# Performance work log

Hardware: AMD Instinct MI355X
Metric: run time of the kernel (lower is better)

The kernel has to match this reference:

```python
import jax, jax.numpy as jnp
import numpy as np

D_MODEL = 1024
NUM_HEADS = 16
D_K = D_MODEL // NUM_HEADS
THETA = 10000.0
BATCH = 4
SEQ = 2048


def _apply_rope(t, positions, theta):
    # t: (B, H, S, d_k); positions: (S,) int
    d_k = t.shape[-1]
    inv_freq = theta ** (-jnp.arange(0, d_k, 2, dtype=jnp.float32) / d_k)  # (d_k/2,)
    angles = positions.astype(jnp.float32)[:, None] * inv_freq[None, :]    # (S, d_k/2)
    cos = jnp.cos(angles)
    sin = jnp.sin(angles)
    x1 = t[..., 0::2]
    x2 = t[..., 1::2]
    r1 = x1 * cos - x2 * sin
    r2 = x1 * sin + x2 * cos
    # interleave back to (..., d_k)
    return jnp.stack([r1, r2], axis=-1).reshape(t.shape)


def setup_inputs() -> dict:
    key = jax.random.key(0)
    k0, k1, k2, k3, k4 = jax.random.split(key, 5)
    scale = 1.0 / np.sqrt(D_MODEL)
    return {
        "x": jax.random.normal(k0, (BATCH, SEQ, D_MODEL), dtype=jnp.float32),
        "wq": jax.random.normal(k1, (D_MODEL, D_MODEL), dtype=jnp.float32) * scale,
        "wk": jax.random.normal(k2, (D_MODEL, D_MODEL), dtype=jnp.float32) * scale,
        "wv": jax.random.normal(k3, (D_MODEL, D_MODEL), dtype=jnp.float32) * scale,
        "wo": jax.random.normal(k4, (D_MODEL, D_MODEL), dtype=jnp.float32) * scale,
        "token_positions": jnp.arange(SEQ, dtype=jnp.int32),
    }


def reference(x, wq, wk, wv, wo, token_positions):
    B, S, _ = x.shape
    H, dk = NUM_HEADS, D_K

    def proj(w):
        # Linear: y = x @ w.T, then split heads -> (B, H, S, d_k)
        y = jnp.einsum("bsd,ed->bse", x, w)
        return y.reshape(B, S, H, dk).transpose(0, 2, 1, 3)

    q = proj(wq)
    k = proj(wk)
    v = proj(wv)

    q = _apply_rope(q, token_positions, THETA)
    k = _apply_rope(k, token_positions, THETA)

    scores = jnp.einsum("bhqd,bhkd->bhqk", q, k) / jnp.sqrt(jnp.float32(dk))
    causal = jnp.tril(jnp.ones((S, S), dtype=bool))  # (S, S)
    scores = jnp.where(causal[None, None, :, :], scores, -jnp.inf)
    attn = jax.nn.softmax(scores, axis=-1)
    out = jnp.einsum("bhqk,bhkd->bhqd", attn, v)        # (B, H, S, d_k)
    out = out.transpose(0, 2, 1, 3).reshape(B, S, H * dk)
    return jnp.einsum("bse,de->bsd", out, wo)
```

## Files before the change

kernel.cpp:

```cpp
#include <hip/hip_runtime.h>
#include <hip/hip_bf16.h>

#define D_MODEL 1024
#define NHEADS 16
#define DKH 64
#define BATCH 4
#define SEQ 2048
#define BH_ (BATCH*NHEADS)
#define MROWS (BATCH*SEQ)

typedef __attribute__((ext_vector_type(8))) short bf16x8;
typedef __attribute__((ext_vector_type(4))) float f32x4;
typedef __attribute__((ext_vector_type(4))) short short4v;

static __device__ __forceinline__ unsigned short f2b(float f){
  union { float f; unsigned u; } v; v.f = f;
  unsigned u = v.u;
  return (unsigned short)((u + 0x7FFFu + ((u >> 16) & 1u)) >> 16);
}
static __device__ __forceinline__ float b2f(unsigned short h){
  union { unsigned u; float f; } v; v.u = ((unsigned)h) << 16; return v.f;
}

static __device__ __forceinline__ f32x4 mfma16(bf16x8 a, bf16x8 b, f32x4 c){
  return __builtin_amdgcn_mfma_f32_16x16x32_bf16(a, b, c, 0, 0, 0);
}

static __device__ __forceinline__ float fexp2(float x){
#if __has_builtin(__builtin_amdgcn_exp2f)
  return __builtin_amdgcn_exp2f(x);
#else
  float r; asm("v_exp_f32 %0, %1" : "=v"(r) : "v"(x)); return r;
#endif
}

static __device__ __forceinline__ void gload_lds16(const unsigned short* g, void* l){
  __builtin_amdgcn_global_load_lds((const __attribute__((address_space(1))) void*)g,
                                   (__attribute__((address_space(3))) void*)l,
                                   16, 0, 0);
}

__global__ void cvt_bf16_kernel(const float* __restrict__ src,
                                unsigned short* __restrict__ dst, int n4){
  int i = blockIdx.x*blockDim.x + threadIdx.x;
  if (i >= n4) return;
  float4 f = ((const float4*)src)[i];
  short4v o;
  o.x = (short)f2b(f.x); o.y = (short)f2b(f.y);
  o.z = (short)f2b(f.z); o.w = (short)f2b(f.w);
  ((short4v*)dst)[i] = o;
}

__global__ void cvt_w_kernel(const float* __restrict__ wq, const float* __restrict__ wk,
                             const float* __restrict__ wv, const float* __restrict__ wo,
                             unsigned short* __restrict__ wcat, unsigned short* __restrict__ wob){
  int i = blockIdx.x*blockDim.x + threadIdx.x;
  int seg = i >> 18;
  int j = i & 0x3FFFF;
  const float* s = (seg==0) ? wq : (seg==1) ? wk : (seg==2) ? wv : wo;
  unsigned short* d = (seg < 3) ? (wcat + ((size_t)seg << 20)) : wob;
  float4 f = ((const float4*)s)[j];
  short4v o;
  o.x = (short)f2b(f.x); o.y = (short)f2b(f.y);
  o.z = (short)f2b(f.z); o.w = (short)f2b(f.w);
  ((short4v*)d)[j] = o;
}

#define BM 128
#define BN 128
#define BKG 64

template<int MODE>
__global__ __launch_bounds__(256, 3) void gemm_nt(const unsigned short* __restrict__ A,
                                                  const unsigned short* __restrict__ Bw,
                                                  void* __restrict__ C,
                                                  int M, int N, int K)
{
  __shared__ unsigned short As[BM*BKG];
  __shared__ unsigned short Bs[BN*BKG];
  const int t = threadIdx.x;
  const int lane = t & 63;
  const int wv = t >> 6;
  const int wr = wv >> 1, wc = wv & 1;
  const int l15 = lane & 15, l4 = lane >> 4;
  const int m0 = blockIdx.y*BM, n0 = blockIdx.x*BN;

  f32x4 acc[4][4] = {};

  const int srow = lane >> 3;
  const int sce  = (lane & 7) * 8;

  for (int kt = 0; kt < K; kt += BKG){
    __syncthreads();
    #pragma unroll
    for (int jj = 0; jj < 4; ++jj){
      const int i = wv + jj*4;
      const int row = i*8 + srow;
      gload_lds16(A  + (size_t)(m0 + row)*K + kt + sce, (char*)As + i*1024 + lane*16);
      gload_lds16(Bw + (size_t)(n0 + row)*K + kt + sce, (char*)Bs + i*1024 + lane*16);
    }
    __syncthreads();
    #pragma unroll
    for (int kk = 0; kk < 2; ++kk){
      bf16x8 af[4], bfr[4];
      #pragma unroll
      for (int mi = 0; mi < 4; ++mi)
        af[mi] = *(const bf16x8*)((const char*)As + (wr*64 + mi*16 + l15)*128 + kk*64 + l4*16);
      #pragma unroll
      for (int ni = 0; ni < 4; ++ni)
        bfr[ni] = *(const bf16x8*)((const char*)Bs + (wc*64 + ni*16 + l15)*128 + kk*64 + l4*16);
      #pragma unroll
      for (int mi = 0; mi < 4; ++mi)
        #pragma unroll
        for (int ni = 0; ni < 4; ++ni)
          acc[mi][ni] = mfma16(af[mi], bfr[ni], acc[mi][ni]);
    }
  }

  #pragma unroll
  for (int mi = 0; mi < 4; ++mi)
    #pragma unroll
    for (int ni = 0; ni < 4; ++ni)
      #pragma unroll
      for (int r = 0; r < 4; ++r){
        int row = m0 + wr*64 + mi*16 + l4*4 + r;
        int col = n0 + wc*64 + ni*16 + l15;
        float v = acc[mi][ni][r];
        if (MODE == 0){
          int which = col >> 10;
          int cl = col & 1023;
          int b = row >> 11, s = row & (SEQ-1);
          int h = cl >> 6,  d = cl & (DKH-1);
          ((unsigned short*)C)[(size_t)which*((size_t)BH_*SEQ*DKH)
                               + ((size_t)(b*NHEADS + h)*SEQ + s)*DKH + d] = f2b(v);
        } else {
          ((float*)C)[(size_t)row*N + col] = v;
        }
      }
}

__global__ void rope_kernel(unsigned int* __restrict__ qk,
                            const int* __restrict__ pos, int npairs){
  int i = blockIdx.x*blockDim.x + threadIdx.x;
  if (i >= npairs) return;
  int j = i & (DKH/2 - 1);
  int s = (i >> 5) & (SEQ-1);
  float p = (float)pos[s];
  float fr = expf(-((float)(2*j) * (1.0f/DKH)) * 9.210340371976184f);
  float ang = p * fr;
  float sn, cs;
  sincosf(ang, &sn, &cs);
  unsigned u = qk[i];
  float x1 = b2f((unsigned short)(u & 0xFFFFu));
  float x2 = b2f((unsigned short)(u >> 16));
  float r1 = x1*cs - x2*sn;
  float r2 = x1*sn + x2*cs;
  qk[i] = (unsigned)f2b(r1) | ((unsigned)f2b(r2) << 16);
}

__global__ void vtrans_kernel(const unsigned short* __restrict__ vin,
                              unsigned short* __restrict__ vt){
  __shared__ unsigned short tile[64][65];
  int bh = blockIdx.y;
  int s0 = blockIdx.x * 64;
  const unsigned short* src = vin + ((size_t)bh*SEQ + s0)*DKH;
  for (int i = threadIdx.x; i < 64*64; i += 256)
    tile[i >> 6][i & 63] = src[(size_t)(i >> 6)*DKH + (i & 63)];
  __syncthreads();
  unsigned short* dst = vt + (size_t)bh*DKH*SEQ + s0;
  for (int i = threadIdx.x; i < 64*64; i += 256)
    dst[(size_t)(i >> 6)*SEQ + (i & 63)] = tile[i & 63][i >> 6];
}

#define QW 32
#define QB 128
#define KVB 64

__global__ __launch_bounds__(256, 2) void attn_kernel(const unsigned short* __restrict__ Q,
                                                      const unsigned short* __restrict__ Kw,
                                                      const unsigned short* __restrict__ Vt,
                                                      unsigned short* __restrict__ Ob)
{
  __shared__ unsigned short Ks[2][KVB*64];
  __shared__ unsigned short Vs[2][KVB*64];
  __shared__ unsigned short Ps[4][QW*KVB];

  const int t = threadIdx.x;
  const int lane = t & 63;
  const int wv = t >> 6;
  const int l15 = lane & 15, l4 = lane >> 4;

  const int bid = blockIdx.x;
  const int bh = bid & (BH_-1);
  const int qt = (SEQ/QB - 1) - (bid >> 6);
  const int q0 = qt * QB;
  const int qw0 = q0 + wv*QW;

  const unsigned short* kg = Kw + (size_t)bh*SEQ*DKH;
  const unsigned short* vg = Vt + (size_t)bh*DKH*SEQ;
  const unsigned short* qg = Q  + ((size_t)bh*SEQ + qw0)*DKH;

  bf16x8 qa[2][2];
  #pragma unroll
  for (int qi = 0; qi < 2; ++qi)
    #pragma unroll
    for (int c = 0; c < 2; ++c)
      qa[qi][c] = *(const bf16x8*)(qg + (qi*16 + l15)*DKH + c*32 + l4*8);

  const float KAPPA = 0.125f * 1.4426950408889634f;
  float m_r[2] = {-1e30f, -1e30f};
  float l_r[2] = {0.f, 0.f};
  f32x4 oacc[2][4] = {};

  const int srow = t >> 3;
  const int scb  = (t & 7) * 16;
  const int sko  = scb ^ ((srow & 7) << 4);
  const size_t vstride = (size_t)SEQ * 2;

  const int ntB   = q0/KVB + 2;
  const int twmax = (qw0 + QW - 1) >> 6;

  bf16x8 kl0, kl1, vl0, vl1;
  {
    const char* ksrc = (const char*)kg;
    const char* vsrc = (const char*)vg;
    kl0 = *(const bf16x8*)(ksrc + srow*128 + sko);
    kl1 = *(const bf16x8*)(ksrc + (srow+32)*128 + sko);
    vl0 = *(const bf16x8*)(vsrc + (size_t)srow*vstride + sko);
    vl1 = *(const bf16x8*)(vsrc + (size_t)(srow+32)*vstride + sko);
    *(bf16x8*)((char*)Ks[0] + srow*128 + scb)      = kl0;
    *(bf16x8*)((char*)Ks[0] + (srow+32)*128 + scb) = kl1;
    *(bf16x8*)((char*)Vs[0] + srow*128 + scb)      = vl0;
    *(bf16x8*)((char*)Vs[0] + (srow+32)*128 + scb) = vl1;
  }

  for (int tt = 0; tt < ntB; ++tt){
    const int cur = tt & 1;
    __syncthreads();
    const bool pre = (tt + 1 < ntB);
    if (pre){
      const size_t kvoff = (size_t)(tt+1) * KVB;
      const char* ksrc = (const char*)kg + kvoff*128;
      const char* vsrc = (const char*)vg + kvoff*2;
      kl0 = *(const bf16x8*)(ksrc + srow*128 + sko);
      kl1 = *(const bf16x8*)(ksrc + (srow+32)*128 + sko);
      vl0 = *(const bf16x8*)(vsrc + (size_t)srow*vstride + sko);
      vl1 = *(const bf16x8*)(vsrc + (size_t)(srow+32)*vstride + sko);
    }

    if (tt <= twmax){
      const char* kb = (const char*)Ks[cur];
      const char* vb = (const char*)Vs[cur];
      char* pb = (char*)Ps[wv];
      const int sw = (l15 & 7) << 4;
      const bool needmask = (tt == twmax);

      f32x4 sacc[4][2];
      #pragma unroll
      for (int kt = 0; kt < 4; ++kt){
        const int krow = kt*16 + l15;
        bf16x8 kf0 = *(const bf16x8*)(kb + krow*128 + ((l4*16) ^ sw));
        bf16x8 kf1 = *(const bf16x8*)(kb + krow*128 + ((64 + l4*16) ^ sw));
        #pragma unroll
        for (int qi = 0; qi < 2; ++qi){
          f32x4 a = {};
          a = mfma16(kf0, qa[qi][0], a);
          a = mfma16(kf1, qa[qi][1], a);
          sacc[kt][qi] = a;
        }
      }

      const int kv0 = tt * KVB;
      #pragma unroll
      for (int qi = 0; qi < 2; ++qi){
        const int qrow = qw0 + qi*16 + l15;
        float p[16];
        float mloc = -1e30f;
        #pragma unroll
        for (int kt = 0; kt < 4; ++kt)
          #pragma unroll
          for (int r = 0; r < 4; ++r){
            float x = sacc[kt][qi][r] * KAPPA;
            if (needmask){
              int kvg = kv0 + kt*16 + l4*4 + r;
              x = (kvg > qrow) ? -1e30f : x;
            }
            p[kt*4+r] = x;
            mloc = fmaxf(mloc, x);
          }
        mloc = fmaxf(mloc, __shfl_xor(mloc, 16));
        mloc = fmaxf(mloc, __shfl_xor(mloc, 32));

        const bool skip = __all(mloc - m_r[qi] <= 12.0f);
        float mn = m_r[qi];
        if (!skip){
          mn = fmaxf(m_r[qi], mloc);
          float alpha = fexp2(m_r[qi] - mn);
          m_r[qi] = mn;
          l_r[qi] *= alpha;
          float ar[4];
          #pragma unroll
          for (int r = 0; r < 4; ++r) ar[r] = __shfl(alpha, l4*4 + r);
          #pragma unroll
          for (int dt = 0; dt < 4; ++dt)
            #pragma unroll
            for (int r = 0; r < 4; ++r) oacc[qi][dt][r] *= ar[r];
        }
        float rs = 0.f;
        #pragma unroll
        for (int i = 0; i < 16; ++i){ p[i] = fexp2(p[i] - mn); rs += p[i]; }
        rs += __shfl_xor(rs, 16);
        rs += __shfl_xor(rs, 32);
        l_r[qi] += rs;

        char* pr = pb + (qi*16 + l15)*128;
        #pragma unroll
        for (int kt = 0; kt < 4; ++kt){
          unsigned u0, u1;
          asm("v_cvt_pk_bf16_f32 %0, %1, %2" : "=v"(u0) : "v"(p[kt*4+0]), "v"(p[kt*4+1]));
          asm("v_cvt_pk_bf16_f32 %0, %1, %2" : "=v"(u1) : "v"(p[kt*4+2]), "v"(p[kt*4+3]));
          unsigned long long uu = (unsigned long long)u0 | ((unsigned long long)u1 << 32);
          *(unsigned long long*)(pr + ((kt*32 + l4*8) ^ sw)) = uu;
        }
      }

      bf16x8 pa[2][2];
      #pragma unroll
      for (int qi = 0; qi < 2; ++qi){
        const char* pr = pb + (qi*16 + l15)*128;
        pa[qi][0] = *(const bf16x8*)(pr + ((l4*16) ^ sw));
        pa[qi][1] = *(const bf16x8*)(pr + ((64 + l4*16) ^ sw));
      }

      #pragma unroll
      for (int dt = 0; dt < 4; ++dt){
        const int vrow = dt*16 + l15;
        bf16x8 vf0 = *(const bf16x8*)(vb + vrow*128 + ((l4*16) ^ sw));
        bf16x8 vf1 = *(const bf16x8*)(vb + vrow*128 + ((64 + l4*16) ^ sw));
        #pragma unroll
        for (int qi = 0; qi < 2; ++qi){
          oacc[qi][dt] = mfma16(pa[qi][0], vf0, oacc[qi][dt]);
          oacc[qi][dt] = mfma16(pa[qi][1], vf1, oacc[qi][dt]);
        }
      }
    }

    if (pre){
      char* kd = (char*)Ks[cur^1];
      char* vd = (char*)Vs[cur^1];
      *(bf16x8*)(kd + srow*128 + scb)      = kl0;
      *(bf16x8*)(kd + (srow+32)*128 + scb) = kl1;
      *(bf16x8*)(vd + srow*128 + scb)      = vl0;
      *(bf16x8*)(vd + (srow+32)*128 + scb) = vl1;
    }
  }

  const int b = bh >> 4, h = bh & 15;
  #pragma unroll
  for (int qi = 0; qi < 2; ++qi){
    float inv = 1.0f / l_r[qi];
    float ir[4];
    #pragma unroll
    for (int r = 0; r < 4; ++r) ir[r] = __shfl(inv, l4*4 + r);
    #pragma unroll
    for (int r = 0; r < 4; ++r){
      int q = qw0 + qi*16 + l4*4 + r;
      unsigned short* orow = Ob + ((size_t)(b*SEQ + q))*D_MODEL + h*DKH;
      #pragma unroll
      for (int dt = 0; dt < 4; ++dt)
        orow[dt*16 + l15] = f2b(oacc[qi][dt][r] * ir[r]);
    }
  }
}

extern "C" void kernel_launch(void* const* d_in, const int* in_sizes, int n_in,
                              void* d_out, int out_size, void* d_ws, size_t ws_size,
                              hipStream_t stream)
{
  const float* x  = (const float*)d_in[0];
  const float* wq = (const float*)d_in[1];
  const float* wk = (const float*)d_in[2];
  const float* wv = (const float*)d_in[3];
  const float* wo = (const float*)d_in[4];
  const int* tp   = (const int*)d_in[5];
  float* out = (float*)d_out;

  unsigned short* ws = (unsigned short*)d_ws;
  size_t off = 0;
  unsigned short* xb   = ws + off; off += (size_t)MROWS*D_MODEL;
  unsigned short* wcat = ws + off; off += (size_t)3*D_MODEL*D_MODEL;
  unsigned short* wob  = ws + off; off += (size_t)D_MODEL*D_MODEL;
  unsigned short* qw   = ws + off; off += (size_t)BH_*SEQ*DKH;
  unsigned short* kw   = ws + off; off += (size_t)BH_*SEQ*DKH;
  unsigned short* vtmp = ws + off; off += (size_t)BH_*SEQ*DKH;
  unsigned short* vt   = ws + off; off += (size_t)BH_*SEQ*DKH;
  unsigned short* ao   = vtmp;

  cvt_bf16_kernel<<<(MROWS*D_MODEL/4 + 255)/256, 256, 0, stream>>>(x, xb, MROWS*D_MODEL/4);
  cvt_w_kernel<<<(4*262144 + 255)/256, 256, 0, stream>>>(wq, wk, wv, wo, wcat, wob);

  gemm_nt<0><<<dim3(3*D_MODEL/BN, MROWS/BM), 256, 0, stream>>>(xb, wcat, qw, MROWS, 3*D_MODEL, D_MODEL);

  const int npairs = BH_*SEQ*(DKH/2);
  rope_kernel<<<(npairs + 255)/256, 256, 0, stream>>>((unsigned int*)qw, tp, npairs);
  rope_kernel<<<(npairs + 255)/256, 256, 0, stream>>>((unsigned int*)kw, tp, npairs);

  vtrans_kernel<<<dim3(SEQ/64, BH_), 256, 0, stream>>>(vtmp, vt);

  attn_kernel<<<BH_*(SEQ/QB), 256, 0, stream>>>(qw, kw, vt, ao);

  gemm_nt<1><<<dim3(D_MODEL/BN, MROWS/BM), 256, 0, stream>>>(ao, wob, out, MROWS, D_MODEL, D_MODEL);
}
```

Before: 282.9 us.

## Fuse RoPE and V transpose into QKV GEMM epilogue using a precomputed trig table

Removes the two standalone RoPE passes and the V transpose kernel. The QKV GEMM epilogue now applies RoPE to Q/K tiles, using a lane shuffle to fetch the paired element and a cos/sin table built once per call. For V tiles it stages the accumulators transposed in a swizzled shared-memory buffer and writes V^T directly. This cuts several full read-modify-write passes over Q, K and V and a few launches, in exchange for a heavier GEMM epilogue. The attention kernel's launch bounds are also raised to 3 blocks per CU, which may increase register pressure.

```diff
diff --git a/kernel.cpp b/kernel.cpp
--- a/kernel.cpp
+++ b/kernel.cpp
@@ -66,6 +66,17 @@
   ((short4v*)d)[j] = o;
 }
 
+__global__ void rope_tab_kernel(const int* __restrict__ pos, float2* __restrict__ tab){
+  int i = blockIdx.x*blockDim.x + threadIdx.x;
+  if (i >= SEQ*32) return;
+  int s = i >> 5, j = i & 31;
+  float p = (float)pos[s];
+  float fr = expf(-((float)(2*j) * (1.0f/DKH)) * 9.210340371976184f);
+  float sn, cs;
+  sincosf(p * fr, &sn, &cs);
+  tab[i] = make_float2(cs, sn);
+}
+
 #define BM 128
 #define BN 128
 #define BKG 64
@@ -74,10 +85,12 @@
 __global__ __launch_bounds__(256, 3) void gemm_nt(const unsigned short* __restrict__ A,
                                                   const unsigned short* __restrict__ Bw,
                                                   void* __restrict__ C,
+                                                  const float2* __restrict__ tab,
                                                   int M, int N, int K)
 {
-  __shared__ unsigned short As[BM*BKG];
-  __shared__ unsigned short Bs[BN*BKG];
+  __shared__ unsigned short smem[BM*BKG + BN*BKG];
+  unsigned short* As = smem;
+  unsigned short* Bs = smem + BM*BKG;
   const int t = threadIdx.x;
   const int lane = t & 63;
   const int wv = t >> 6;
@@ -117,66 +130,86 @@
     }
   }
 
+  if (MODE == 1){
+    #pragma unroll
+    for (int mi = 0; mi < 4; ++mi)
+      #pragma unroll
+      for (int ni = 0; ni < 4; ++ni)
+        #pragma unroll
+        for (int r = 0; r < 4; ++r){
+          int row = m0 + wr*64 + mi*16 + l4*4 + r;
+          int col = n0 + wc*64 + ni*16 + l15;
+          ((float*)C)[(size_t)row*N + col] = acc[mi][ni][r];
+        }
+    return;
+  }
+
+  const int which = n0 >> 10;
+
+  if (which == 2){
+    __syncthreads();
+    #pragma unroll
+    for (int mi = 0; mi < 4; ++mi)
+      #pragma unroll
+      for (int ni = 0; ni < 4; ++ni){
+        int d_l = wc*64 + ni*16 + l15;
+        int s0  = wr*64 + mi*16 + l4*4;
+        short4v pk;
+        pk.x = (short)f2b(acc[mi][ni][0]);
+        pk.y = (short)f2b(acc[mi][ni][1]);
+        pk.z = (short)f2b(acc[mi][ni][2]);
+        pk.w = (short)f2b(acc[mi][ni][3]);
+        int byte = d_l*256 + ((s0*2) ^ ((d_l & 7) << 4));
+        *(short4v*)((char*)smem + byte) = pk;
+      }
+    __syncthreads();
+    const int d_l = t >> 1;
+    const int half = t & 1;
+    const int hb = (n0 & 1023) >> 6;
+    const int b = m0 >> 11;
+    const int s_b = m0 & (SEQ-1);
+    const int bh = b*NHEADS + hb + (d_l >> 6);
+    const int d = d_l & 63;
+    unsigned short* vt = (unsigned short*)C + 2*((size_t)BH_*SEQ*DKH);
+    unsigned short* dst = vt + ((size_t)bh*DKH + d)*SEQ + s_b + half*64;
+    #pragma unroll
+    for (int c = 0; c < 8; ++c){
+      int sl = half*64 + c*8;
+      int byte = d_l*256 + ((sl*2) ^ ((d_l & 7) << 4));
+      *(bf16x8*)(dst + c*8) = *(const bf16x8*)((const char*)smem + byte);
+    }
+    return;
+  }
+
+  unsigned short* qk = (unsigned short*)C + (size_t)which*((size_t)BH_*SEQ*DKH);
   #pragma unroll
-  for (int mi = 0; mi < 4; ++mi)
-    #pragma unroll
-    for (int ni = 0; ni < 4; ++ni)
+  for (int ni = 0; ni < 4; ++ni){
+    int col = n0 + wc*64 + ni*16 + l15;
+    int cl = col & 1023;
+    int h = cl >> 6, dd = cl & (DKH-1);
+    int j = dd >> 1;
+    bool odd = dd & 1;
+    #pragma unroll
+    for (int mi = 0; mi < 4; ++mi)
       #pragma unroll
       for (int r = 0; r < 4; ++r){
         int row = m0 + wr*64 + mi*16 + l4*4 + r;
-        int col = n0 + wc*64 + ni*16 + l15;
-        float v = acc[mi][ni][r];
-        if (MODE == 0){
-          int which = col >> 10;
-          int cl = col & 1023;
-          int b = row >> 11, s = row & (SEQ-1);
-          int h = cl >> 6,  d = cl & (DKH-1);
-          ((unsigned short*)C)[(size_t)which*((size_t)BH_*SEQ*DKH)
-                               + ((size_t)(b*NHEADS + h)*SEQ + s)*DKH + d] = f2b(v);
-        } else {
-          ((float*)C)[(size_t)row*N + col] = v;
-        }
-      }
-}
-
-__global__ void rope_kernel(unsigned int* __restrict__ qk,
-                            const int* __restrict__ pos, int npairs){
-  int i = blockIdx.x*blockDim.x + threadIdx.x;
-  if (i >= npairs) return;
-  int j = i & (DKH/2 - 1);
-  int s = (i >> 5) & (SEQ-1);
-  float p = (float)pos[s];
-  float fr = expf(-((float)(2*j) * (1.0f/DKH)) * 9.210340371976184f);
-  float ang = p * fr;
-  float sn, cs;
-  sincosf(ang, &sn, &cs);
-  unsigned u = qk[i];
-  float x1 = b2f((unsigned short)(u & 0xFFFFu));
-  float x2 = b2f((unsigned short)(u >> 16));
-  float r1 = x1*cs - x2*sn;
-  float r2 = x1*sn + x2*cs;
-  qk[i] = (unsigned)f2b(r1) | ((unsigned)f2b(r2) << 16);
-}
-
-__global__ void vtrans_kernel(const unsigned short* __restrict__ vin,
-                              unsigned short* __restrict__ vt){
-  __shared__ unsigned short tile[64][65];
-  int bh = blockIdx.y;
-  int s0 = blockIdx.x * 64;
-  const unsigned short* src = vin + ((size_t)bh*SEQ + s0)*DKH;
-  for (int i = threadIdx.x; i < 64*64; i += 256)
-    tile[i >> 6][i & 63] = src[(size_t)(i >> 6)*DKH + (i & 63)];
-  __syncthreads();
-  unsigned short* dst = vt + (size_t)bh*DKH*SEQ + s0;
-  for (int i = threadIdx.x; i < 64*64; i += 256)
-    dst[(size_t)(i >> 6)*SEQ + (i & 63)] = tile[i & 63][i >> 6];
+        int b = row >> 11, s = row & (SEQ-1);
+        float2 cst = tab[s*32 + j];
+        float xv = acc[mi][ni][r];
+        float pv = __shfl_xor(xv, 1);
+        float res = odd ? fmaf(xv, cst.x,  pv*cst.y)
+                        : fmaf(xv, cst.x, -pv*cst.y);
+        qk[((size_t)(b*NHEADS + h)*SEQ + s)*DKH + dd] = f2b(res);
+      }
+  }
 }
 
 #define QW 32
 #define QB 128
 #define KVB 64
 
-__global__ __launch_bounds__(256, 2) void attn_kernel(const unsigned short* __restrict__ Q,
+__global__ __launch_bounds__(256, 3) void attn_kernel(const unsigned short* __restrict__ Q,
                                                       const unsigned short* __restrict__ Kw,
                                                       const unsigned short* __restrict__ Vt,
                                                       unsigned short* __restrict__ Ob)
@@ -392,22 +425,19 @@
   unsigned short* wob  = ws + off; off += (size_t)D_MODEL*D_MODEL;
   unsigned short* qw   = ws + off; off += (size_t)BH_*SEQ*DKH;
   unsigned short* kw   = ws + off; off += (size_t)BH_*SEQ*DKH;
-  unsigned short* vtmp = ws + off; off += (size_t)BH_*SEQ*DKH;
   unsigned short* vt   = ws + off; off += (size_t)BH_*SEQ*DKH;
-  unsigned short* ao   = vtmp;
+  unsigned short* ao   = ws + off; off += (size_t)BH_*SEQ*DKH;
+  float2* tab = (float2*)(ws + off); off += (size_t)SEQ*32*4;
 
   cvt_bf16_kernel<<<(MROWS*D_MODEL/4 + 255)/256, 256, 0, stream>>>(x, xb, MROWS*D_MODEL/4);
   cvt_w_kernel<<<(4*262144 + 255)/256, 256, 0, stream>>>(wq, wk, wv, wo, wcat, wob);
-
-  gemm_nt<0><<<dim3(3*D_MODEL/BN, MROWS/BM), 256, 0, stream>>>(xb, wcat, qw, MROWS, 3*D_MODEL, D_MODEL);
-
-  const int npairs = BH_*SEQ*(DKH/2);
-  rope_kernel<<<(npairs + 255)/256, 256, 0, stream>>>((unsigned int*)qw, tp, npairs);
-  rope_kernel<<<(npairs + 255)/256, 256, 0, stream>>>((unsigned int*)kw, tp, npairs);
-
-  vtrans_kernel<<<dim3(SEQ/64, BH_), 256, 0, stream>>>(vtmp, vt);
+  rope_tab_kernel<<<(SEQ*32 + 255)/256, 256, 0, stream>>>(tp, tab);
+
+  gemm_nt<0><<<dim3(3*D_MODEL/BN, MROWS/BM), 256, 0, stream>>>(xb, wcat, qw, tab,
+                                                               MROWS, 3*D_MODEL, D_MODEL);
 
   attn_kernel<<<BH_*(SEQ/QB), 256, 0, stream>>>(qw, kw, vt, ao);
 
-  gemm_nt<1><<<dim3(D_MODEL/BN, MROWS/BM), 256, 0, stream>>>(ao, wob, out, MROWS, D_MODEL, D_MODEL);
-}
+  gemm_nt<1><<<dim3(D_MODEL/BN, MROWS/BM), 256, 0, stream>>>(ao, wob, out, nullptr,
+                                                             MROWS, D_MODEL, D_MODEL);
+}
```

New measurement: 260.5 us. 1.09x faster.
